# Kernel optimization log

Measured on AMD Instinct MI355X. Metric: run time of the kernel, lower is better.

## Reference

```python
import jax, jax.numpy as jnp
import numpy as np

EPS = 1e-5
LEAK = 0.1
NPOINT = 4096
NSAMPLE = 32


def setup_inputs() -> dict:
    key = jax.random.key(0)
    ks = jax.random.split(key, 6)
    B, N, Cin = 2, 16384, 64
    ch = [Cin + 3, 64, 64, 128]
    xyz = jax.random.normal(ks[0], (B, 3, N), jnp.float32)
    points = jax.random.normal(ks[1], (B, Cin, N), jnp.float32)
    W0 = jax.random.normal(ks[2], (ch[1], ch[0]), jnp.float32) * 0.05
    W1 = jax.random.normal(ks[3], (ch[2], ch[1]), jnp.float32) * 0.05
    W2 = jax.random.normal(ks[4], (ch[3], ch[2]), jnp.float32) * 0.05
    return dict(
        xyz=xyz, points=points, W0=W0, W1=W1, W2=W2,
        g0=jnp.ones((ch[1],), jnp.float32), b0=jnp.zeros((ch[1],), jnp.float32),
        g1=jnp.ones((ch[2],), jnp.float32), b1=jnp.zeros((ch[2],), jnp.float32),
        g2=jnp.ones((ch[3],), jnp.float32), b2=jnp.zeros((ch[3],), jnp.float32),
    )


def _mlp_bn_act(x, W, g, b):
    # 1x1 conv (no bias) + BatchNorm2d (training: batch stats, biased var) + LeakyReLU(0.1)
    x = jnp.einsum('oc,bcsk->bosk', W, x)
    m = jnp.mean(x, axis=(0, 2, 3), keepdims=True)
    v = jnp.mean(jnp.square(x - m), axis=(0, 2, 3), keepdims=True)
    x = (x - m) * jax.lax.rsqrt(v + EPS) * g[None, :, None, None] + b[None, :, None, None]
    return jnp.where(x >= 0, x, LEAK * x)


def reference(xyz, points, W0, W1, W2, g0, b0, g1, b1, g2, b2):
    B, _, N = xyz.shape
    xyz_t = jnp.transpose(xyz, (0, 2, 1))            # [B,N,3]
    new_xyz = xyz[:, :, :NPOINT]                     # [B,3,S]  (use_fps=False path)
    new_xyz_t = jnp.transpose(new_xyz, (0, 2, 1))    # [B,S,3]

    # squared distances [B,S,N]
    d = (jnp.sum(new_xyz_t ** 2, -1)[:, :, None]
         + jnp.sum(xyz_t ** 2, -1)[:, None, :]
         - 2.0 * jnp.einsum('bsc,bnc->bsn', new_xyz_t, xyz_t))
    _, knn_idx = jax.lax.top_k(-d, NSAMPLE)          # [B,S,K] nearest neighbors

    gather = jax.vmap(lambda arr, idx: arr[idx])     # ([N,C],[S,K]) -> [S,K,C]
    neighbor_xyz = gather(xyz_t, knn_idx)            # [B,S,K,3]
    direction = neighbor_xyz - new_xyz_t[:, :, None, :]
    grouped = gather(jnp.transpose(points, (0, 2, 1)), knn_idx)  # [B,S,K,Cin]

    x = jnp.transpose(jnp.concatenate([direction, grouped], -1), (0, 3, 1, 2))  # [B,Cin+3,S,K]
    x = _mlp_bn_act(x, W0, g0, b0)
    x = _mlp_bn_act(x, W1, g1, b1)
    x = _mlp_bn_act(x, W2, g2, b2)
    new_points = jnp.max(x, axis=-1)                 # [B,128,S] max-pool over nsample
    return new_xyz, new_points
```

## Files before the change

### kernel.cpp

```cpp
#include <hip/hip_runtime.h>
#include <hip/hip_bf16.h>
#include <stdint.h>

#define N_ALL   16384
#define NPOINT  4096
#define KNN_K   32
#define BATCH   2
#define P_TOT   (BATCH*NPOINT*KNN_K)
#define P_TOTF  262144.0f
#define EPSV    1e-5f

typedef __attribute__((ext_vector_type(8))) short bf16x8;
typedef __attribute__((ext_vector_type(4))) float f32x4;

__device__ unsigned short g_knn[P_TOT];
__device__ __attribute__((aligned(16))) float g_pxyzn[BATCH*N_ALL*4];
__device__ __attribute__((aligned(16))) short g_ptb[BATCH*N_ALL*64];
__device__ __attribute__((aligned(16))) short g_x0b[(size_t)P_TOT*64];
__device__ __attribute__((aligned(16))) short g_x1b[(size_t)P_TOT*64];
__device__ __attribute__((aligned(16))) short g_x2b[(size_t)P_TOT*128];
__device__ __attribute__((aligned(16))) float g_mx[(size_t)BATCH*NPOINT*128];
__device__ __attribute__((aligned(16))) float g_mn[(size_t)BATCH*NPOINT*128];
__device__ __attribute__((aligned(16))) short g_Wb0[4*3*64*8];
__device__ __attribute__((aligned(16))) short g_Wb1[4*2*64*8];
__device__ __attribute__((aligned(16))) short g_Wb2[8*2*64*8];
__device__ float g_part0[128], g_part1[128], g_part2[256];

__device__ __forceinline__ float b2f(short s) {
  union { unsigned u; float f; } v; v.u = ((unsigned)(unsigned short)s) << 16; return v.f;
}
__device__ __forceinline__ short f2b(float f) {
  union { float f; unsigned u; } v; v.f = f;
  unsigned u = v.u;
  u += 0x7FFFu + ((u >> 16) & 1u);
  return (short)(u >> 16);
}
__device__ __forceinline__ unsigned pkbf(float a, float b) {
  union { __hip_bfloat162 h; unsigned u; } v;
  v.h = __float22bfloat162_rn(make_float2(a, b));
  return v.u;
}
__device__ __forceinline__ unsigned long long bperm64(unsigned long long v, int byteaddr) {
  int lo = __builtin_amdgcn_ds_bpermute(byteaddr, (int)(unsigned)(v & 0xFFFFFFFFULL));
  int hi = __builtin_amdgcn_ds_bpermute(byteaddr, (int)(unsigned)(v >> 32));
  return (((unsigned long long)(unsigned)hi) << 32) | (unsigned)lo;
}
__device__ __forceinline__ unsigned long long u64min(unsigned long long a, unsigned long long b) {
  return a < b ? a : b;
}
__device__ __forceinline__ unsigned long long selstage(unsigned long long v,
                                                       unsigned long long pv, bool mx) {
  bool lt = v < pv;
  return (lt != mx) ? v : pv;
}

__device__ __forceinline__ void knn_merge32(unsigned long long& vL,
                                            unsigned long long& worst,
                                            unsigned& worst_hi, float& wd,
                                            unsigned long long vB, int hl,
                                            int aX1, int aX2, int aX4, int aX8,
                                            int aX16, int aRev, int aW) {
  vB = selstage(vB, bperm64(vB, aX1),  ((hl & 1) != 0) != ((hl & 2) != 0));
  vB = selstage(vB, bperm64(vB, aX2),  ((hl & 2) != 0) != ((hl & 4) != 0));
  vB = selstage(vB, bperm64(vB, aX1),  ((hl & 1) != 0) != ((hl & 4) != 0));
  vB = selstage(vB, bperm64(vB, aX4),  ((hl & 4) != 0) != ((hl & 8) != 0));
  vB = selstage(vB, bperm64(vB, aX2),  ((hl & 2) != 0) != ((hl & 8) != 0));
  vB = selstage(vB, bperm64(vB, aX1),  ((hl & 1) != 0) != ((hl & 8) != 0));
  vB = selstage(vB, bperm64(vB, aX8),  ((hl & 8) != 0) != ((hl & 16) != 0));
  vB = selstage(vB, bperm64(vB, aX4),  ((hl & 4) != 0) != ((hl & 16) != 0));
  vB = selstage(vB, bperm64(vB, aX2),  ((hl & 2) != 0) != ((hl & 16) != 0));
  vB = selstage(vB, bperm64(vB, aX1),  ((hl & 1) != 0) != ((hl & 16) != 0));
  vB = selstage(vB, bperm64(vB, aX16), (hl & 16) != 0);
  vB = selstage(vB, bperm64(vB, aX8),  (hl & 8) != 0);
  vB = selstage(vB, bperm64(vB, aX4),  (hl & 4) != 0);
  vB = selstage(vB, bperm64(vB, aX2),  (hl & 2) != 0);
  vB = selstage(vB, bperm64(vB, aX1),  (hl & 1) != 0);
  vL = u64min(vL, bperm64(vB, aRev));
  vL = selstage(vL, bperm64(vL, aX16), (hl & 16) != 0);
  vL = selstage(vL, bperm64(vL, aX8),  (hl & 8) != 0);
  vL = selstage(vL, bperm64(vL, aX4),  (hl & 4) != 0);
  vL = selstage(vL, bperm64(vL, aX2),  (hl & 2) != 0);
  vL = selstage(vL, bperm64(vL, aX1),  (hl & 1) != 0);
  worst = bperm64(vL, aW);
  worst_hi = (unsigned)(worst >> 32);
  unsigned wh = worst_hi;
  unsigned ub = (wh & 0x80000000u) ? (wh ^ 0x80000000u) : ~wh;
  wd = (wh == 0xFFFFFFFFu) ? __builtin_inff() : __uint_as_float(ub);
}

__global__ __launch_bounds__(256) void k_setup(const float* __restrict__ xyz,
                                               const float* __restrict__ points,
                                               const float* __restrict__ W0,
                                               const float* __restrict__ W1,
                                               const float* __restrict__ W2,
                                               float* __restrict__ out) {
#pragma clang fp contract(off)
  __shared__ float tile[64][65];
  int blk = blockIdx.x;
  int t = threadIdx.x;
  if (blk < 512) {
    int b  = blk >> 8;
    int n0 = (blk & 255) << 6;
#pragma unroll
    for (int r = 0; r < 16; r++) {
      int lin = r * 256 + t;
      int c = lin >> 6, nn = lin & 63;
      tile[c][nn] = points[((size_t)(b * 64 + c)) * N_ALL + n0 + nn];
    }
    __syncthreads();
#pragma unroll
    for (int r = 0; r < 16; r++) {
      int lin = r * 256 + t;
      int nn = lin >> 6, c = lin & 63;
      g_ptb[((size_t)(b * N_ALL + n0 + nn)) * 64 + c] = f2b(tile[c][nn]);
    }
  } else if (blk < 640) {
    int i = (blk - 512) * 256 + t;
    if (i < 24576) {
      int s = i & 4095;
      int c = (i >> 12) % 3;
      int b = i / 12288;
      out[i] = xyz[(b * 3 + c) * N_ALL + s];
    }
    int b = i >> 14, n = i & 16383;
    const float* xb = xyz + b * 3 * N_ALL;
    float x = xb[n], y = xb[N_ALL + n], z = xb[2 * N_ALL + n];
    float4 p; p.x = x; p.y = y; p.z = z; p.w = x * x + y * y + z * z;
    ((float4*)g_pxyzn)[i] = p;
  } else {
    for (int i = t; i < 4 * 3 * 64 * 8; i += 256) {
      int j = i & 7, lane = (i >> 3) & 63, rest = i >> 9;
      int kt = rest % 3, mt = rest / 3;
      int m = 16 * mt + (lane & 15);
      int k = 32 * kt + (lane >> 4) * 8 + j;
      float v = 0.f;
      if (k < 64) v = W0[m * 67 + 3 + k];
      else if (k < 67) v = W0[m * 67 + (k - 64)];
      g_Wb0[i] = f2b(v);
    }
    for (int i = t; i < 4 * 2 * 64 * 8; i += 256) {
      int j = i & 7, lane = (i >> 3) & 63;
      int kt = (i >> 9) & 1, mt = i >> 10;
      int m = 16 * mt + (lane & 15);
      int k = 32 * kt + (lane >> 4) * 8 + j;
      g_Wb1[i] = f2b(W1[m * 64 + k]);
    }
    for (int i = t; i < 8 * 2 * 64 * 8; i += 256) {
      int j = i & 7, lane = (i >> 3) & 63;
      int kt = (i >> 9) & 1, mt = i >> 10;
      int m = 16 * mt + (lane & 15);
      int k = 32 * kt + (lane >> 4) * 8 + j;
      g_Wb2[i] = f2b(W2[m * 64 + k]);
    }
    if (t < 128) { g_part0[t] = 0.f; g_part1[t] = 0.f; }
    g_part2[t] = 0.f;
  }
}

__global__ __launch_bounds__(256, 8) void k_knn() {
#pragma clang fp contract(off)
  __shared__ unsigned long long buf[4][2][64];
  int wv = threadIdx.x >> 6;
  int lane = threadIdx.x & 63;
  int half = lane >> 5;
  int hl = lane & 31;
  int lanebase = lane & 32;
  unsigned long long* bufh = buf[wv][half];

  int qpair = wv >> 1;
  int range = wv & 1;
  int q = blockIdx.x * 4 + qpair * 2 + half;
  int b = q >> 12, s = q & 4095;
  const float4* pb = (const float4*)g_pxyzn + (b << 14);
  float4 qp = pb[s];
  float qx = qp.x, qy = qp.y, qz = qp.z, qn = qp.w;

  int aX1  = (lanebase | (hl ^ 1))  << 2;
  int aX2  = (lanebase | (hl ^ 2))  << 2;
  int aX4  = (lanebase | (hl ^ 4))  << 2;
  int aX8  = (lanebase | (hl ^ 8))  << 2;
  int aX16 = (lanebase | (hl ^ 16)) << 2;
  int aRev = (lanebase | (31 - hl)) << 2;
  int aW   = (lanebase | 31)        << 2;

  unsigned long long vL = ~0ULL;
  unsigned long long worst = ~0ULL;
  unsigned worst_hi = 0xFFFFFFFFu;
  float wd = __builtin_inff();
  int F = 0;

  int base = range << 13;
  for (int n0 = base; n0 < base + 8192; n0 += 128) {
    float4 p0 = pb[n0 + hl];
    float4 p1 = pb[n0 + 32 + hl];
    float4 p2 = pb[n0 + 64 + hl];
    float4 p3 = pb[n0 + 96 + hl];
    float d[4];
    {
      float dt0 = (qx * p0.x + qy * p0.y) + qz * p0.z;
      float dt1 = (qx * p1.x + qy * p1.y) + qz * p1.z;
      float dt2 = (qx * p2.x + qy * p2.y) + qz * p2.z;
      float dt3 = (qx * p3.x + qy * p3.y) + qz * p3.z;
      d[0] = __builtin_fmaf(-2.0f, dt0, qn + p0.w);
      d[1] = __builtin_fmaf(-2.0f, dt1, qn + p1.w);
      d[2] = __builtin_fmaf(-2.0f, dt2, qn + p2.w);
      d[3] = __builtin_fmaf(-2.0f, dt3, qn + p3.w);
    }
    float md = fminf(fminf(d[0], d[1]), fminf(d[2], d[3]));
    if (__ballot(md <= wd)) {
#pragma unroll
      for (int t = 0; t < 4; t++) {
        bool sv = d[t] <= wd;
        unsigned long long bl = __ballot(sv);
        unsigned mb = half ? (unsigned)(bl >> 32) : (unsigned)bl;
        if (sv) {
          unsigned u = __float_as_uint(d[t]);
          u ^= ((unsigned)(((int)u) >> 31)) | 0x80000000u;
          unsigned long long c = (((unsigned long long)u) << 32)
                               | (unsigned)(n0 + 32 * t + hl);
          bufh[F + __popc(mb & ((1u << hl) - 1u))] = c;
        }
        F += __popc(mb);
        if (__ballot(F >= 32)) {
          int take = F >= 32 ? 32 : F;
          unsigned long long vB = (hl < take) ? bufh[hl] : ~0ULL;
          knn_merge32(vL, worst, worst_hi, wd, vB, hl,
                      aX1, aX2, aX4, aX8, aX16, aRev, aW);
          int R = F - take;
          if (hl < R) bufh[hl] = bufh[32 + hl];
          F = R;
        }
      }
    }
  }
  if (__ballot(F > 0)) {
    unsigned long long vB = (hl < F) ? bufh[hl] : ~0ULL;
    knn_merge32(vL, worst, worst_hi, wd, vB, hl, aX1, aX2, aX4, aX8, aX16, aRev, aW);
  }

  bufh[hl] = vL;
  __syncthreads();
  unsigned long long vB = buf[wv ^ 1][half][hl];
  vL = u64min(vL, bperm64(vB, aRev));
  vL = selstage(vL, bperm64(vL, aX16), (hl & 16) != 0);
  vL = selstage(vL, bperm64(vL, aX8),  (hl & 8) != 0);
  vL = selstage(vL, bperm64(vL, aX4),  (hl & 4) != 0);
  vL = selstage(vL, bperm64(vL, aX2),  (hl & 2) != 0);
  vL = selstage(vL, bperm64(vL, aX1),  (hl & 1) != 0);
  if (range == 0)
    g_knn[((size_t)q << 5) | hl] = (unsigned short)(vL & 0xFFFF);
}

__global__ __launch_bounds__(256) void k_l0(const float* __restrict__ xyz) {
  __shared__ short feats[256][104];
  int t = threadIdx.x;
  int p0 = blockIdx.x * 256;
  {
    int p = p0 + t;
    int idx = g_knn[p];
    int s = (p >> 5) & 4095;
    int b = p >> 17;
    const short* src = g_ptb + ((size_t)((b << 14) + idx) << 6);
#pragma unroll
    for (int i = 0; i < 8; i++)
      ((int4*)&feats[t][0])[i] = ((const int4*)src)[i];
    const float* xb = xyz + b * 3 * N_ALL;
    int4 z; z.x = 0; z.y = 0; z.z = 0; z.w = 0;
    *(int4*)&feats[t][64] = z;
    *(int4*)&feats[t][72] = z;
    *(int4*)&feats[t][80] = z;
    *(int4*)&feats[t][88] = z;
    short4 d3;
    d3.x = f2b(xb[idx] - xb[s]);
    d3.y = f2b(xb[N_ALL + idx] - xb[N_ALL + s]);
    d3.z = f2b(xb[2 * N_ALL + idx] - xb[2 * N_ALL + s]);
    d3.w = 0;
    *(short4*)&feats[t][64] = d3;
  }
  __syncthreads();
  int lane = t & 63, wv = t >> 6;
  int l15 = lane & 15, quad = lane >> 4;
  bf16x8 A[4][3];
#pragma unroll
  for (int mt = 0; mt < 4; mt++)
#pragma unroll
    for (int kt = 0; kt < 3; kt++)
      A[mt][kt] = *(const bf16x8*)(g_Wb0 + (((mt * 3 + kt) * 64 + lane) << 3));
  f32x4 C[4][4];
#pragma unroll
  for (int mt = 0; mt < 4; mt++)
#pragma unroll
    for (int nt = 0; nt < 4; nt++) C[mt][nt] = 0.f;
#pragma unroll
  for (int kt = 0; kt < 3; kt++)
#pragma unroll
    for (int nt = 0; nt < 4; nt++) {
      bf16x8 B = *(const bf16x8*)(&feats[wv * 64 + nt * 16 + l15][kt * 32 + quad * 8]);
#pragma unroll
      for (int mt = 0; mt < 4; mt++)
        C[mt][nt] = __builtin_amdgcn_mfma_f32_16x16x32_bf16(A[mt][kt], B, C[mt][nt], 0, 0, 0);
    }
#pragma unroll
  for (int mt = 0; mt < 4; mt++)
#pragma unroll
    for (int nt = 0; nt < 4; nt++) {
      int p = p0 + wv * 64 + nt * 16 + l15;
      int c0 = mt * 16 + quad * 4;
      uint2 o;
      o.x = pkbf(C[mt][nt][0], C[mt][nt][1]);
      o.y = pkbf(C[mt][nt][2], C[mt][nt][3]);
      *(uint2*)(g_x0b + ((size_t)p << 6) + c0) = o;
    }
}

__global__ __launch_bounds__(256) void k_l1(const float* __restrict__ g0,
                                            const float* __restrict__ b0) {
  __shared__ float scA[64], shA[64];
  int t = threadIdx.x;
  if (t < 64) {
    float m = g_part0[t] / P_TOTF;
    float v = g_part0[64 + t] / P_TOTF - m * m;
    float sc = g0[t] / sqrtf(v + EPSV);
    scA[t] = sc; shA[t] = b0[t] - m * sc;
  }
  __syncthreads();
  int lane = t & 63, wv = t >> 6;
  int l15 = lane & 15, quad = lane >> 4;
  int p0 = blockIdx.x * 256 + wv * 64;
  float scv[2][8], shv[2][8];
#pragma unroll
  for (int kt = 0; kt < 2; kt++)
#pragma unroll
    for (int j = 0; j < 8; j++) {
      int c = kt * 32 + quad * 8 + j;
      scv[kt][j] = scA[c]; shv[kt][j] = shA[c];
    }
  bf16x8 A[4][2];
#pragma unroll
  for (int mt = 0; mt < 4; mt++)
#pragma unroll
    for (int kt = 0; kt < 2; kt++)
      A[mt][kt] = *(const bf16x8*)(g_Wb1 + (((mt * 2 + kt) * 64 + lane) << 3));
  f32x4 C[4][4];
#pragma unroll
  for (int mt = 0; mt < 4; mt++)
#pragma unroll
    for (int nt = 0; nt < 4; nt++) C[mt][nt] = 0.f;
#pragma unroll
  for (int kt = 0; kt < 2; kt++)
#pragma unroll
    for (int nt = 0; nt < 4; nt++) {
      const short* src = g_x0b + (((size_t)(p0 + nt * 16 + l15)) << 6) + kt * 32 + quad * 8;
      uint4 raw = *(const uint4*)src;
      bf16x8 B;
      unsigned* Bu = (unsigned*)&B;
      unsigned ru[4] = {raw.x, raw.y, raw.z, raw.w};
#pragma unroll
      for (int jj = 0; jj < 4; jj++) {
        float lo = __uint_as_float(ru[jj] << 16);
        float hi = __uint_as_float(ru[jj] & 0xFFFF0000u);
        float a0 = lo * scv[kt][2*jj]   + shv[kt][2*jj];
        float a1 = hi * scv[kt][2*jj+1] + shv[kt][2*jj+1];
        a0 = fmaxf(a0, 0.1f * a0);
        a1 = fmaxf(a1, 0.1f * a1);
        Bu[jj] = pkbf(a0, a1);
      }
#pragma unroll
      for (int mt = 0; mt < 4; mt++)
        C[mt][nt] = __builtin_amdgcn_mfma_f32_16x16x32_bf16(A[mt][kt], B, C[mt][nt], 0, 0, 0);
    }
#pragma unroll
  for (int mt = 0; mt < 4; mt++)
#pragma unroll
    for (int nt = 0; nt < 4; nt++) {
      int p = p0 + nt * 16 + l15;
      int c0 = mt * 16 + quad * 4;
      uint2 o;
      o.x = pkbf(C[mt][nt][0], C[mt][nt][1]);
      o.y = pkbf(C[mt][nt][2], C[mt][nt][3]);
      *(uint2*)(g_x1b + ((size_t)p << 6) + c0) = o;
    }
}

__global__ __launch_bounds__(256) void k_l2(const float* __restrict__ g1,
                                            const float* __restrict__ b1) {
  __shared__ float scA[64], shA[64];
  int t = threadIdx.x;
  if (t < 64) {
    float m = g_part1[t] / P_TOTF;
    float v = g_part1[64 + t] / P_TOTF - m * m;
    float sc = g1[t] / sqrtf(v + EPSV);
    scA[t] = sc; shA[t] = b1[t] - m * sc;
  }
  __syncthreads();
  int lane = t & 63, wv = t >> 6;
  int l15 = lane & 15, quad = lane >> 4;
  int chh = wv & 1;
  int p0 = blockIdx.x * 128 + (wv >> 1) * 64;
  float scv[2][8], shv[2][8];
#pragma unroll
  for (int kt = 0; kt < 2; kt++)
#pragma unroll
    for (int j = 0; j < 8; j++) {
      int c = kt * 32 + quad * 8 + j;
      scv[kt][j] = scA[c]; shv[kt][j] = shA[c];
    }
  bf16x8 A[4][2];
#pragma unroll
  for (int mt = 0; mt < 4; mt++)
#pragma unroll
    for (int kt = 0; kt < 2; kt++)
      A[mt][kt] = *(const bf16x8*)(g_Wb2 + ((((4 * chh + mt) * 2 + kt) * 64 + lane) << 3));
  f32x4 C[4][4];
#pragma unroll
  for (int mt = 0; mt < 4; mt++)
#pragma unroll
    for (int nt = 0; nt < 4; nt++) C[mt][nt] = 0.f;
#pragma unroll
  for (int kt = 0; kt < 2; kt++)
#pragma unroll
    for (int nt = 0; nt < 4; nt++) {
      const short* src = g_x1b + (((size_t)(p0 + nt * 16 + l15)) << 6) + kt * 32 + quad * 8;
      uint4 raw = *(const uint4*)src;
      bf16x8 B;
      unsigned* Bu = (unsigned*)&B;
      unsigned ru[4] = {raw.x, raw.y, raw.z, raw.w};
#pragma unroll
      for (int jj = 0; jj < 4; jj++) {
        float lo = __uint_as_float(ru[jj] << 16);
        float hi = __uint_as_float(ru[jj] & 0xFFFF0000u);
        float a0 = lo * scv[kt][2*jj]   + shv[kt][2*jj];
        float a1 = hi * scv[kt][2*jj+1] + shv[kt][2*jj+1];
        a0 = fmaxf(a0, 0.1f * a0);
        a1 = fmaxf(a1, 0.1f * a1);
        Bu[jj] = pkbf(a0, a1);
      }
#pragma unroll
      for (int mt = 0; mt < 4; mt++)
        C[mt][nt] = __builtin_amdgcn_mfma_f32_16x16x32_bf16(A[mt][kt], B, C[mt][nt], 0, 0, 0);
    }
#pragma unroll
  for (int mt = 0; mt < 4; mt++)
#pragma unroll
    for (int nt = 0; nt < 4; nt++) {
      int p = p0 + nt * 16 + l15;
      int c0 = (4 * chh + mt) * 16 + quad * 4;
      uint2 o;
      o.x = pkbf(C[mt][nt][0], C[mt][nt][1]);
      o.y = pkbf(C[mt][nt][2], C[mt][nt][3]);
      *(uint2*)(g_x2b + ((size_t)p << 7) + c0) = o;
    }
}

__global__ __launch_bounds__(1024) void k_red64(const short* __restrict__ x,
                                                float* __restrict__ part) {
  __shared__ float sm[64][68], sq[64][68];
  int t = threadIdx.x;
  int cl = t & 15, pr = t >> 4;
  float s0 = 0.f, s1 = 0.f, s2 = 0.f, s3 = 0.f;
  float q0 = 0.f, q1 = 0.f, q2 = 0.f, q3 = 0.f;
  int pbase = blockIdx.x * 1024;
  for (int i = 0; i < 16; i++) {
    int p = pbase + pr + i * 64;
    uint2 d = *(const uint2*)(x + ((size_t)p << 6) + cl * 4);
    float a0 = __uint_as_float(d.x << 16);
    float a1 = __uint_as_float(d.x & 0xFFFF0000u);
    float a2 = __uint_as_float(d.y << 16);
    float a3 = __uint_as_float(d.y & 0xFFFF0000u);
    s0 += a0; q0 = fmaf(a0, a0, q0);
    s1 += a1; q1 = fmaf(a1, a1, q1);
    s2 += a2; q2 = fmaf(a2, a2, q2);
    s3 += a3; q3 = fmaf(a3, a3, q3);
  }
  float4 vs; vs.x = s0; vs.y = s1; vs.z = s2; vs.w = s3;
  float4 vq; vq.x = q0; vq.y = q1; vq.z = q2; vq.w = q3;
  *(float4*)&sm[pr][cl * 4] = vs;
  *(float4*)&sq[pr][cl * 4] = vq;
  __syncthreads();
  if (t < 64) {
    float S = 0.f, Q = 0.f;
#pragma unroll
    for (int r = 0; r < 64; r++) { S += sm[r][t]; Q += sq[r][t]; }
    atomicAdd(part + t, S); atomicAdd(part + 64 + t, Q);
  }
}

__global__ __launch_bounds__(1024) void k_red128mx(const short* __restrict__ x,
                                                   float* __restrict__ part) {
  __shared__ float sm[32][132], sq[32][132];
  int t = threadIdx.x;
  int cl = t & 31, wv = t >> 5;
  int g = blockIdx.x * 32 + wv;
  size_t pbase = (size_t)g << 5;
  float s0 = 0.f, s1 = 0.f, s2 = 0.f, s3 = 0.f;
  float q0 = 0.f, q1 = 0.f, q2 = 0.f, q3 = 0.f;
  float mx0 = -3.4e38f, mn0 = 3.4e38f, mx1 = -3.4e38f, mn1 = 3.4e38f;
  float mx2 = -3.4e38f, mn2 = 3.4e38f, mx3 = -3.4e38f, mn3 = 3.4e38f;
#pragma unroll
  for (int k = 0; k < 32; k++) {
    uint2 d = *(const uint2*)(x + ((pbase + k) << 7) + cl * 4);
    float a0 = __uint_as_float(d.x << 16);
    float a1 = __uint_as_float(d.x & 0xFFFF0000u);
    float a2 = __uint_as_float(d.y << 16);
    float a3 = __uint_as_float(d.y & 0xFFFF0000u);
    s0 += a0; q0 = fmaf(a0, a0, q0);
    s1 += a1; q1 = fmaf(a1, a1, q1);
    s2 += a2; q2 = fmaf(a2, a2, q2);
    s3 += a3; q3 = fmaf(a3, a3, q3);
    mx0 = fmaxf(mx0, a0); mn0 = fminf(mn0, a0);
    mx1 = fmaxf(mx1, a1); mn1 = fminf(mn1, a1);
    mx2 = fmaxf(mx2, a2); mn2 = fminf(mn2, a2);
    mx3 = fmaxf(mx3, a3); mn3 = fminf(mn3, a3);
  }
  float4 vmx; vmx.x = mx0; vmx.y = mx1; vmx.z = mx2; vmx.w = mx3;
  float4 vmn; vmn.x = mn0; vmn.y = mn1; vmn.z = mn2; vmn.w = mn3;
  *(float4*)(g_mx + ((size_t)g << 7) + cl * 4) = vmx;
  *(float4*)(g_mn + ((size_t)g << 7) + cl * 4) = vmn;
  float4 vs; vs.x = s0; vs.y = s1; vs.z = s2; vs.w = s3;
  float4 vq; vq.x = q0; vq.y = q1; vq.z = q2; vq.w = q3;
  *(float4*)&sm[wv][cl * 4] = vs;
  *(float4*)&sq[wv][cl * 4] = vq;
  __syncthreads();
  if (t < 128) {
    float S = 0.f, Q = 0.f;
#pragma unroll
    for (int r = 0; r < 32; r++) { S += sm[r][t]; Q += sq[r][t]; }
    atomicAdd(part + t, S); atomicAdd(part + 128 + t, Q);
  }
}

__global__ __launch_bounds__(256) void k_epi(const float* __restrict__ g2,
                                             const float* __restrict__ b2,
                                             float* __restrict__ out) {
  __shared__ float scA[128], shA[128];
  __shared__ float res[16][132];
  int t = threadIdx.x;
  if (t < 128) {
    float m = g_part2[t] / P_TOTF;
    float v = g_part2[128 + t] / P_TOTF - m * m;
    float sc = g2[t] / sqrtf(v + EPSV);
    scA[t] = sc; shA[t] = b2[t] - m * sc;
  }
  __syncthreads();
  int cp = t & 63, sl = t >> 6;
  int c0 = cp * 2, c1 = c0 + 1;
  float sc0 = scA[c0], sh0 = shA[c0];
  float sc1 = scA[c1], sh1 = shA[c1];
  int sg0 = blockIdx.x * 16;
  for (int it = 0; it < 4; it++) {
    int sgl = sl * 4 + it;
    size_t off = ((size_t)(sg0 + sgl) << 7) + c0;
    float2 vmx = *(const float2*)(g_mx + off);
    float2 vmn = *(const float2*)(g_mn + off);
    float a0 = (sc0 >= 0.f ? vmx.x : vmn.x) * sc0 + sh0; a0 = fmaxf(a0, 0.1f * a0);
    float a1 = (sc1 >= 0.f ? vmx.y : vmn.y) * sc1 + sh1; a1 = fmaxf(a1, 0.1f * a1);
    res[sgl][c0] = a0; res[sgl][c1] = a1;
  }
  __syncthreads();
  int b = sg0 >> 12, s0 = sg0 & 4095;
#pragma unroll
  for (int w = 0; w < 2; w++) {
    int fidx = t * 2 + w;
    int c = fidx >> 2, qi = fidx & 3;
    float4 o;
    o.x = res[qi * 4 + 0][c];
    o.y = res[qi * 4 + 1][c];
    o.z = res[qi * 4 + 2][c];
    o.w = res[qi * 4 + 3][c];
    *(float4*)(out + 24576 + (((size_t)(b * 128 + c)) << 12) + s0 + qi * 4) = o;
  }
}

extern "C" void kernel_launch(void* const* d_in, const int* in_sizes, int n_in,
                              void* d_out, int out_size, void* d_ws, size_t ws_size,
                              hipStream_t stream) {
  (void)in_sizes; (void)n_in; (void)out_size; (void)d_ws; (void)ws_size;
  const float* xyz    = (const float*)d_in[0];
  const float* points = (const float*)d_in[1];
  const float* W0     = (const float*)d_in[2];
  const float* W1     = (const float*)d_in[3];
  const float* W2     = (const float*)d_in[4];
  const float* g0     = (const float*)d_in[5];
  const float* b0     = (const float*)d_in[6];
  const float* g1     = (const float*)d_in[7];
  const float* b1     = (const float*)d_in[8];
  const float* g2     = (const float*)d_in[9];
  const float* b2     = (const float*)d_in[10];
  float* out = (float*)d_out;

  short *x0b, *x1b, *x2b; float *part0, *part1, *part2;
  hipGetSymbolAddress((void**)&x0b,   HIP_SYMBOL(g_x0b));
  hipGetSymbolAddress((void**)&x1b,   HIP_SYMBOL(g_x1b));
  hipGetSymbolAddress((void**)&x2b,   HIP_SYMBOL(g_x2b));
  hipGetSymbolAddress((void**)&part0, HIP_SYMBOL(g_part0));
  hipGetSymbolAddress((void**)&part1, HIP_SYMBOL(g_part1));
  hipGetSymbolAddress((void**)&part2, HIP_SYMBOL(g_part2));

  hipLaunchKernelGGL(k_setup,    dim3(641),  dim3(256),  0, stream, xyz, points, W0, W1, W2, out);
  hipLaunchKernelGGL(k_knn,      dim3(2048), dim3(256),  0, stream);
  hipLaunchKernelGGL(k_l0,       dim3(1024), dim3(256),  0, stream, xyz);
  hipLaunchKernelGGL(k_red64,    dim3(256),  dim3(1024), 0, stream, x0b, part0);
  hipLaunchKernelGGL(k_l1,       dim3(1024), dim3(256),  0, stream, g0, b0);
  hipLaunchKernelGGL(k_red64,    dim3(256),  dim3(1024), 0, stream, x1b, part1);
  hipLaunchKernelGGL(k_l2,       dim3(2048), dim3(256),  0, stream, g1, b1);
  hipLaunchKernelGGL(k_red128mx, dim3(256),  dim3(1024), 0, stream, x2b, part2);
  hipLaunchKernelGGL(k_epi,      dim3(512),  dim3(256),  0, stream, g2, b2, out);
}
```

Before: 312.2 us.

## Fuse BatchNorm statistics reduction into layer 0 and layer 1 GEMM epilogues

Removes the two standalone k_red64 launches and instead accumulates per-channel sum and sum-of-squares of the rounded bf16 outputs inside k_l0 and k_l1, then reduces them in shared memory and atomically adds into partial buffers. The atomics are spread over four slots selected by block index to reduce contention, and the consuming kernels sum the four slots. This avoids rereading the x0 and x1 activations from global memory and saves two launches. The cost is extra registers, shared memory and a block-level reduction in the GEMM kernels, which may lower occupancy.

Result: faster. 301.9 us (-3.3%).

```diff
diff --git a/kernel.cpp b/kernel.cpp
--- a/kernel.cpp
+++ b/kernel.cpp
@@ -24,7 +24,9 @@
 __device__ __attribute__((aligned(16))) short g_Wb0[4*3*64*8];
 __device__ __attribute__((aligned(16))) short g_Wb1[4*2*64*8];
 __device__ __attribute__((aligned(16))) short g_Wb2[8*2*64*8];
-__device__ float g_part0[128], g_part1[128], g_part2[256];
+__device__ float g_p0s[4][128];
+__device__ float g_p1s[4][128];
+__device__ float g_part2[256];
 
 __device__ __forceinline__ float b2f(short s) {
   union { unsigned u; float f; } v; v.u = ((unsigned)(unsigned short)s) << 16; return v.f;
@@ -152,7 +154,9 @@
       int k = 32 * kt + (lane >> 4) * 8 + j;
       g_Wb2[i] = f2b(W2[m * 64 + k]);
     }
-    if (t < 128) { g_part0[t] = 0.f; g_part1[t] = 0.f; }
+    float* z0 = &g_p0s[0][0];
+    float* z1 = &g_p1s[0][0];
+    for (int i = t; i < 512; i += 256) { z0[i] = 0.f; z1[i] = 0.f; }
     g_part2[t] = 0.f;
   }
 }
@@ -252,7 +256,7 @@
 }
 
 __global__ __launch_bounds__(256) void k_l0(const float* __restrict__ xyz) {
-  __shared__ short feats[256][104];
+  __shared__ __attribute__((aligned(16))) short feats[256][104];
   int t = threadIdx.x;
   int p0 = blockIdx.x * 256;
   {
@@ -300,6 +304,9 @@
       for (int mt = 0; mt < 4; mt++)
         C[mt][nt] = __builtin_amdgcn_mfma_f32_16x16x32_bf16(A[mt][kt], B, C[mt][nt], 0, 0, 0);
     }
+  float sA[16], qA[16];
+#pragma unroll
+  for (int i = 0; i < 16; i++) { sA[i] = 0.f; qA[i] = 0.f; }
 #pragma unroll
   for (int mt = 0; mt < 4; mt++)
 #pragma unroll
@@ -310,16 +317,55 @@
       o.x = pkbf(C[mt][nt][0], C[mt][nt][1]);
       o.y = pkbf(C[mt][nt][2], C[mt][nt][3]);
       *(uint2*)(g_x0b + ((size_t)p << 6) + c0) = o;
-    }
+      float v0 = __uint_as_float(o.x << 16);
+      float v1 = __uint_as_float(o.x & 0xFFFF0000u);
+      float v2 = __uint_as_float(o.y << 16);
+      float v3 = __uint_as_float(o.y & 0xFFFF0000u);
+      int ib = mt * 4;
+      sA[ib+0] += v0; qA[ib+0] = fmaf(v0, v0, qA[ib+0]);
+      sA[ib+1] += v1; qA[ib+1] = fmaf(v1, v1, qA[ib+1]);
+      sA[ib+2] += v2; qA[ib+2] = fmaf(v2, v2, qA[ib+2]);
+      sA[ib+3] += v3; qA[ib+3] = fmaf(v3, v3, qA[ib+3]);
+    }
+  __syncthreads();
+  float* red = (float*)&feats[0][0];
+  int rb = t * 36;
+#pragma unroll
+  for (int w = 0; w < 4; w++) {
+    float4 vs; vs.x = sA[w*4+0]; vs.y = sA[w*4+1]; vs.z = sA[w*4+2]; vs.w = sA[w*4+3];
+    float4 vq; vq.x = qA[w*4+0]; vq.y = qA[w*4+1]; vq.z = qA[w*4+2]; vq.w = qA[w*4+3];
+    *(float4*)&red[rb + w*4] = vs;
+    *(float4*)&red[rb + 16 + w*4] = vq;
+  }
+  __syncthreads();
+  if (t < 64) {
+    int qd = (t >> 2) & 3;
+    int i = ((t >> 4) << 2) | (t & 3);
+    float S = 0.f, Q = 0.f;
+#pragma unroll
+    for (int w = 0; w < 4; w++)
+#pragma unroll
+      for (int l = 0; l < 16; l++) {
+        int row = (w * 64 + qd * 16 + l) * 36;
+        S += red[row + i];
+        Q += red[row + 16 + i];
+      }
+    float* sh = &g_p0s[blockIdx.x & 3][0];
+    atomicAdd(sh + t, S);
+    atomicAdd(sh + 64 + t, Q);
+  }
 }
 
 __global__ __launch_bounds__(256) void k_l1(const float* __restrict__ g0,
                                             const float* __restrict__ b0) {
   __shared__ float scA[64], shA[64];
+  __shared__ __attribute__((aligned(16))) float red[256 * 36];
   int t = threadIdx.x;
   if (t < 64) {
-    float m = g_part0[t] / P_TOTF;
-    float v = g_part0[64 + t] / P_TOTF - m * m;
+    float ps = g_p0s[0][t] + g_p0s[1][t] + g_p0s[2][t] + g_p0s[3][t];
+    float pq = g_p0s[0][64+t] + g_p0s[1][64+t] + g_p0s[2][64+t] + g_p0s[3][64+t];
+    float m = ps / P_TOTF;
+    float v = pq / P_TOTF - m * m;
     float sc = g0[t] / sqrtf(v + EPSV);
     scA[t] = sc; shA[t] = b0[t] - m * sc;
   }
@@ -369,6 +415,9 @@
       for (int mt = 0; mt < 4; mt++)
         C[mt][nt] = __builtin_amdgcn_mfma_f32_16x16x32_bf16(A[mt][kt], B, C[mt][nt], 0, 0, 0);
     }
+  float sA[16], qA[16];
+#pragma unroll
+  for (int i = 0; i < 16; i++) { sA[i] = 0.f; qA[i] = 0.f; }
 #pragma unroll
   for (int mt = 0; mt < 4; mt++)
 #pragma unroll
@@ -379,7 +428,41 @@
       o.x = pkbf(C[mt][nt][0], C[mt][nt][1]);
       o.y = pkbf(C[mt][nt][2], C[mt][nt][3]);
       *(uint2*)(g_x1b + ((size_t)p << 6) + c0) = o;
-    }
+      float v0 = __uint_as_float(o.x << 16);
+      float v1 = __uint_as_float(o.x & 0xFFFF0000u);
+      float v2 = __uint_as_float(o.y << 16);
+      float v3 = __uint_as_float(o.y & 0xFFFF0000u);
+      int ib = mt * 4;
+      sA[ib+0] += v0; qA[ib+0] = fmaf(v0, v0, qA[ib+0]);
+      sA[ib+1] += v1; qA[ib+1] = fmaf(v1, v1, qA[ib+1]);
+      sA[ib+2] += v2; qA[ib+2] = fmaf(v2, v2, qA[ib+2]);
+      sA[ib+3] += v3; qA[ib+3] = fmaf(v3, v3, qA[ib+3]);
+    }
+  int rb = t * 36;
+#pragma unroll
+  for (int w = 0; w < 4; w++) {
+    float4 vs; vs.x = sA[w*4+0]; vs.y = sA[w*4+1]; vs.z = sA[w*4+2]; vs.w = sA[w*4+3];
+    float4 vq; vq.x = qA[w*4+0]; vq.y = qA[w*4+1]; vq.z = qA[w*4+2]; vq.w = qA[w*4+3];
+    *(float4*)&red[rb + w*4] = vs;
+    *(float4*)&red[rb + 16 + w*4] = vq;
+  }
+  __syncthreads();
+  if (t < 64) {
+    int qd = (t >> 2) & 3;
+    int i = ((t >> 4) << 2) | (t & 3);
+    float S = 0.f, Q = 0.f;
+#pragma unroll
+    for (int w = 0; w < 4; w++)
+#pragma unroll
+      for (int l = 0; l < 16; l++) {
+        int row = (w * 64 + qd * 16 + l) * 36;
+        S += red[row + i];
+        Q += red[row + 16 + i];
+      }
+    float* sh = &g_p1s[blockIdx.x & 3][0];
+    atomicAdd(sh + t, S);
+    atomicAdd(sh + 64 + t, Q);
+  }
 }
 
 __global__ __launch_bounds__(256) void k_l2(const float* __restrict__ g1,
@@ -387,8 +470,10 @@
   __shared__ float scA[64], shA[64];
   int t = threadIdx.x;
   if (t < 64) {
-    float m = g_part1[t] / P_TOTF;
-    float v = g_part1[64 + t] / P_TOTF - m * m;
+    float ps = g_p1s[0][t] + g_p1s[1][t] + g_p1s[2][t] + g_p1s[3][t];
+    float pq = g_p1s[0][64+t] + g_p1s[1][64+t] + g_p1s[2][64+t] + g_p1s[3][64+t];
+    float m = ps / P_TOTF;
+    float v = pq / P_TOTF - m * m;
     float sc = g1[t] / sqrtf(v + EPSV);
     scA[t] = sc; shA[t] = b1[t] - m * sc;
   }
@@ -450,39 +535,6 @@
       o.y = pkbf(C[mt][nt][2], C[mt][nt][3]);
       *(uint2*)(g_x2b + ((size_t)p << 7) + c0) = o;
     }
-}
-
-__global__ __launch_bounds__(1024) void k_red64(const short* __restrict__ x,
-                                                float* __restrict__ part) {
-  __shared__ float sm[64][68], sq[64][68];
-  int t = threadIdx.x;
-  int cl = t & 15, pr = t >> 4;
-  float s0 = 0.f, s1 = 0.f, s2 = 0.f, s3 = 0.f;
-  float q0 = 0.f, q1 = 0.f, q2 = 0.f, q3 = 0.f;
-  int pbase = blockIdx.x * 1024;
-  for (int i = 0; i < 16; i++) {
-    int p = pbase + pr + i * 64;
-    uint2 d = *(const uint2*)(x + ((size_t)p << 6) + cl * 4);
-    float a0 = __uint_as_float(d.x << 16);
-    float a1 = __uint_as_float(d.x & 0xFFFF0000u);
-    float a2 = __uint_as_float(d.y << 16);
-    float a3 = __uint_as_float(d.y & 0xFFFF0000u);
-    s0 += a0; q0 = fmaf(a0, a0, q0);
-    s1 += a1; q1 = fmaf(a1, a1, q1);
-    s2 += a2; q2 = fmaf(a2, a2, q2);
-    s3 += a3; q3 = fmaf(a3, a3, q3);
-  }
-  float4 vs; vs.x = s0; vs.y = s1; vs.z = s2; vs.w = s3;
-  float4 vq; vq.x = q0; vq.y = q1; vq.z = q2; vq.w = q3;
-  *(float4*)&sm[pr][cl * 4] = vs;
-  *(float4*)&sq[pr][cl * 4] = vq;
-  __syncthreads();
-  if (t < 64) {
-    float S = 0.f, Q = 0.f;
-#pragma unroll
-    for (int r = 0; r < 64; r++) { S += sm[r][t]; Q += sq[r][t]; }
-    atomicAdd(part + t, S); atomicAdd(part + 64 + t, Q);
-  }
 }
 
 __global__ __launch_bounds__(1024) void k_red128mx(const short* __restrict__ x,
@@ -588,20 +640,14 @@
   const float* b2     = (const float*)d_in[10];
   float* out = (float*)d_out;
 
-  short *x0b, *x1b, *x2b; float *part0, *part1, *part2;
-  hipGetSymbolAddress((void**)&x0b,   HIP_SYMBOL(g_x0b));
-  hipGetSymbolAddress((void**)&x1b,   HIP_SYMBOL(g_x1b));
+  short *x2b; float *part2;
   hipGetSymbolAddress((void**)&x2b,   HIP_SYMBOL(g_x2b));
-  hipGetSymbolAddress((void**)&part0, HIP_SYMBOL(g_part0));
-  hipGetSymbolAddress((void**)&part1, HIP_SYMBOL(g_part1));
   hipGetSymbolAddress((void**)&part2, HIP_SYMBOL(g_part2));
 
   hipLaunchKernelGGL(k_setup,    dim3(641),  dim3(256),  0, stream, xyz, points, W0, W1, W2, out);
   hipLaunchKernelGGL(k_knn,      dim3(2048), dim3(256),  0, stream);
   hipLaunchKernelGGL(k_l0,       dim3(1024), dim3(256),  0, stream, xyz);
-  hipLaunchKernelGGL(k_red64,    dim3(256),  dim3(1024), 0, stream, x0b, part0);
   hipLaunchKernelGGL(k_l1,       dim3(1024), dim3(256),  0, stream, g0, b0);
-  hipLaunchKernelGGL(k_red64,    dim3(256),  dim3(1024), 0, stream, x1b, part1);
   hipLaunchKernelGGL(k_l2,       dim3(2048), dim3(256),  0, stream, g1, b1);
   hipLaunchKernelGGL(k_red128mx, dim3(256),  dim3(1024), 0, stream, x2b, part2);
   hipLaunchKernelGGL(k_epi,      dim3(512),  dim3(256),  0, stream, g2, b2, out);
```
